# Performance work log

Hardware: AMD Instinct MI355X
Metric: run time of the kernel (lower is better)

The kernel has to match this reference:

```python
import jax, jax.numpy as jnp
import numpy as np

TAU = 0.07
COS_EPS = 1e-8   # torch F.cosine_similarity eps
L1_EPS = 1e-12   # torch F.normalize eps
MM_EPS = 1e-8    # min-max renorm eps

B, C, H, W = 64, 256, 32, 32
S, D = 512, 256


def setup_inputs() -> dict:
    key = jax.random.key(0)
    k1, k2, k3, k4 = jax.random.split(key, 4)
    scale = 1.0 / np.sqrt(D)
    return {
        "image_patches": jax.random.normal(k1, (B, C, H, W), dtype=jnp.float32),
        "text_tokens": jax.random.normal(k2, (B, S, D), dtype=jnp.float32),
        "Wv": jax.random.normal(k3, (D, D), dtype=jnp.float32) * scale,
        "bv": jnp.zeros((D,), dtype=jnp.float32),
        "Wt": jax.random.normal(k4, (D, D), dtype=jnp.float32) * scale,
        "bt": jnp.zeros((D,), dtype=jnp.float32),
    }


def _linear(x, Wgt, b):
    return x @ Wgt.T + b


def _l2n(x, axis=-1):
    n = jnp.maximum(jnp.linalg.norm(x, axis=axis, keepdims=True), COS_EPS)
    return x / n


def _sym_ce_diag(sim):
    # sim [..., N, N]; mean of -log_softmax diagonals along both class axes
    lsm_r = jax.nn.log_softmax(sim, axis=-1)
    lsm_c = jax.nn.log_softmax(sim, axis=-2)
    d_r = jnp.diagonal(lsm_r, axis1=-2, axis2=-1)
    d_c = jnp.diagonal(lsm_c, axis1=-2, axis2=-1)
    return 0.5 * (-jnp.mean(d_r) - jnp.mean(d_c))


def reference(image_patches, text_tokens, Wv, bv, Wt, bt):
    b, c, h, w = image_patches.shape
    hw = h * w
    # b c h w -> b (h w) c, then adapters
    patches = image_patches.reshape(b, c, hw).transpose(0, 2, 1)  # [b, hw, c]
    patches = _linear(patches, Wv, bv)          # [b, hw, d]
    tokens = _linear(text_tokens, Wt, bt)       # [b, s, d]

    # global embeddings: mean-pool then adapter (adapter applied twice on vision path)
    g_img = _linear(jnp.mean(patches, axis=1), Wv, bv)  # [b, d]
    g_txt = _linear(jnp.mean(tokens, axis=1), Wt, bt)   # [b, d]

    # global contrastive loss (cosine sim / tau, symmetric CE over batch)
    g_sim = (_l2n(g_img) @ _l2n(g_txt).T) / TAU         # [b, b]
    global_loss = _sym_ce_diag(g_sim)

    # fine-grained alignment
    sim = jnp.einsum('bpd,bsd->bps', patches, tokens)   # [b, hw, s]
    mn = jnp.min(sim, axis=1, keepdims=True)
    mx = jnp.max(sim, axis=1, keepdims=True)
    sim = (sim - mn) / (mx - mn + MM_EPS)
    sigma = 1.0 / hw
    sim = jnp.where(sim < sigma, 0.0, sim)
    # L1 normalize over patch dim (torch F.normalize p=1 dim=1)
    weights = sim / jnp.maximum(jnp.sum(jnp.abs(sim), axis=1, keepdims=True), L1_EPS)
    lgve = jnp.einsum('bps,bpd->bsd', weights, patches)  # [b, s, d]

    # fine-grained contrastive loss: cosine sim between grouped-vision and text tokens
    f_sim = jnp.einsum('bid,bjd->bij', _l2n(lgve), _l2n(tokens)) / TAU  # [b, s, s]
    fine_loss = _sym_ce_diag(f_sim)

    return global_loss + fine_loss
```

## Files before the change

kernel.cpp:

```cpp
#include <hip/hip_runtime.h>
#include <math.h>

#define BB   64
#define HWP  1024
#define SS   512
#define DD   256
#define TAU_INV (1.0f/0.07f)
#define SIGMA   (1.0f/1024.0f)

typedef unsigned short us;
typedef __attribute__((ext_vector_type(8))) short short8v;
typedef __attribute__((ext_vector_type(8))) unsigned short ushort8v;
typedef __attribute__((ext_vector_type(4))) float floatx4;

__device__ __forceinline__ float bf2f(us u) {
    return __uint_as_float((unsigned)u << 16);
}
__device__ __forceinline__ us f2bf(float f) {
    unsigned u = __float_as_uint(f);
    u += 0x7FFFu + ((u >> 16) & 1u);
    return (us)(u >> 16);
}
__device__ __forceinline__ void split_bf(float v, us& h, us& l) {
    h = f2bf(v);
    l = f2bf(v - bf2f(h));
}

__global__ void zero_out_k(float* out) { if (threadIdx.x == 0) out[0] = 0.0f; }

enum { OPM_F32_ROW = 0, OPM_F32_COL = 1, OPM_SPL_ROW = 2, OPM_SPL_COL = 3,
       OPM_B16_COL = 4, OPM_B16_ROW = 5, OPM_WGT_COL = 6 };
enum { OUT_F32 = 0, OUT_B16 = 1 };

#define LDSTRIDE 40

template<int MODE>
__device__ __forceinline__ void stage_tile(
    const char* p0, const char* p1, int ld, int row0, int k0,
    us* ldsH, us* ldsL, int tid,
    const float* wlo, const float* whi)
{
    if constexpr (MODE == OPM_SPL_ROW) {
        const us* ph = (const us*)p0;
        const us* pl = (const us*)p1;
        const int i = tid >> 1, ko = (tid & 1) * 16;
        const long long g = (long long)(row0 + i) * ld + k0 + ko;
        *(ushort8v*)&ldsH[i * LDSTRIDE + ko]     = *(const ushort8v*)&ph[g];
        *(ushort8v*)&ldsH[i * LDSTRIDE + ko + 8] = *(const ushort8v*)&ph[g + 8];
        *(ushort8v*)&ldsL[i * LDSTRIDE + ko]     = *(const ushort8v*)&pl[g];
        *(ushort8v*)&ldsL[i * LDSTRIDE + ko + 8] = *(const ushort8v*)&pl[g + 8];
    } else if constexpr (MODE == OPM_B16_ROW) {
        const us* ph = (const us*)p0;
        const int i = tid >> 1, ko = (tid & 1) * 16;
        const long long g = (long long)(row0 + i) * ld + k0 + ko;
        *(ushort8v*)&ldsH[i * LDSTRIDE + ko]     = *(const ushort8v*)&ph[g];
        *(ushort8v*)&ldsH[i * LDSTRIDE + ko + 8] = *(const ushort8v*)&ph[g + 8];
    } else if constexpr (MODE == OPM_F32_ROW) {
        const float* pf = (const float*)p0;
        const int i = tid >> 1, ko = (tid & 1) * 16;
        const long long g = (long long)(row0 + i) * ld + k0 + ko;
        us h16[16], l16[16];
        #pragma unroll
        for (int c = 0; c < 16; c += 4) {
            float4 v = *(const float4*)&pf[g + c];
            split_bf(v.x, h16[c+0], l16[c+0]); split_bf(v.y, h16[c+1], l16[c+1]);
            split_bf(v.z, h16[c+2], l16[c+2]); split_bf(v.w, h16[c+3], l16[c+3]);
        }
        *(ushort8v*)&ldsH[i * LDSTRIDE + ko]     = *(const ushort8v*)&h16[0];
        *(ushort8v*)&ldsH[i * LDSTRIDE + ko + 8] = *(const ushort8v*)&h16[8];
        *(ushort8v*)&ldsL[i * LDSTRIDE + ko]     = *(const ushort8v*)&l16[0];
        *(ushort8v*)&ldsL[i * LDSTRIDE + ko + 8] = *(const ushort8v*)&l16[8];
    } else if constexpr (MODE == OPM_F32_COL) {
        const float* pf = (const float*)p0;
        const int m = tid & 127, kh = (tid >> 7) * 16;
        const long long base = (long long)(k0 + kh) * ld + row0 + m;
        us vh[16], vl[16];
        #pragma unroll
        for (int kk = 0; kk < 16; ++kk)
            split_bf(pf[base + (long long)kk * ld], vh[kk], vl[kk]);
        *(ushort8v*)&ldsH[m * LDSTRIDE + kh]     = *(const ushort8v*)&vh[0];
        *(ushort8v*)&ldsH[m * LDSTRIDE + kh + 8] = *(const ushort8v*)&vh[8];
        *(ushort8v*)&ldsL[m * LDSTRIDE + kh]     = *(const ushort8v*)&vl[0];
        *(ushort8v*)&ldsL[m * LDSTRIDE + kh + 8] = *(const ushort8v*)&vl[8];
    } else if constexpr (MODE == OPM_B16_COL) {
        const us* ph = (const us*)p0;
        const int m = tid & 127, kh = (tid >> 7) * 16;
        const long long base = (long long)(k0 + kh) * ld + row0 + m;
        us v[16];
        #pragma unroll
        for (int kk = 0; kk < 16; ++kk)
            v[kk] = ph[base + (long long)kk * ld];
        *(ushort8v*)&ldsH[m * LDSTRIDE + kh]     = *(const ushort8v*)&v[0];
        *(ushort8v*)&ldsH[m * LDSTRIDE + kh + 8] = *(const ushort8v*)&v[8];
    } else if constexpr (MODE == OPM_WGT_COL) {
        const us* ph = (const us*)p0;
        const int m = tid & 127, kh = (tid >> 7) * 16;
        const float lo = wlo[row0 + m];
        const float inv = 1.0f / (whi[row0 + m] - lo + 1e-8f);
        const long long base = (long long)(k0 + kh) * ld + row0 + m;
        us v[16];
        #pragma unroll
        for (int kk = 0; kk < 16; ++kk) {
            const float w = (bf2f(ph[base + (long long)kk * ld]) - lo) * inv;
            v[kk] = (w < SIGMA) ? (us)0 : f2bf(w);
        }
        *(ushort8v*)&ldsH[m * LDSTRIDE + kh]     = *(const ushort8v*)&v[0];
        *(ushort8v*)&ldsH[m * LDSTRIDE + kh + 8] = *(const ushort8v*)&v[8];
    }
}

template<int AMODE, int BMODE, int OMODE, int EPI>
__global__ __launch_bounds__(256) void mfma_gemm(
    const void* A0, const void* A1, const void* B0, const void* B1,
    void* C0,
    int M, int N, int K, int lda, int ldb, int ldc,
    long long sA, long long sB, long long sC,
    const float* __restrict__ bias, const float* __restrict__ invm,
    const float* __restrict__ invn, float scale,
    const float* __restrict__ wlo, const float* __restrict__ whi)
{
    constexpr bool ASPL = (AMODE <= OPM_SPL_COL);
    constexpr bool BSPL = (BMODE <= OPM_SPL_COL);
    constexpr int ASZ = 128 * LDSTRIDE;
    __shared__ __align__(16) us Ah[ASZ];
    __shared__ __align__(16) us Al[ASPL ? ASZ : 8];
    __shared__ __align__(16) us Bh[ASZ];
    __shared__ __align__(16) us Bl[BSPL ? ASZ : 8];

    const int tid = threadIdx.x;
    const int w = tid >> 6, lane = tid & 63;
    const int quad = lane >> 4, l16 = lane & 15;
    const int m0 = blockIdx.x * 128, n0 = blockIdx.y * 128;
    const int b = blockIdx.z;

    const char* Ab0 = (const char*)A0 + (long long)b * sA;
    const char* Ab1 = A1 ? (const char*)A1 + (long long)b * sA : nullptr;
    const char* Bb0 = (const char*)B0 + (long long)b * sB;
    const char* Bb1 = B1 ? (const char*)B1 + (long long)b * sB : nullptr;
    const float* wloA = wlo ? wlo + (long long)b * M : nullptr;
    const float* whiA = whi ? whi + (long long)b * M : nullptr;

    floatx4 acc[2][8];
    #pragma unroll
    for (int mi = 0; mi < 2; ++mi)
        #pragma unroll
        for (int ni = 0; ni < 8; ++ni)
            acc[mi][ni] = (floatx4){0.f, 0.f, 0.f, 0.f};

    for (int k0 = 0; k0 < K; k0 += 32) {
        stage_tile<AMODE>(Ab0, Ab1, lda, m0, k0, Ah, Al, tid, wloA, whiA);
        stage_tile<BMODE>(Bb0, Bb1, ldb, n0, k0, Bh, Bl, tid, nullptr, nullptr);
        __syncthreads();

        short8v ah[2], al[2], bh[8], bl[8];
        #pragma unroll
        for (int mi = 0; mi < 2; ++mi) {
            const int r = (32 * w + 16 * mi + l16) * LDSTRIDE + quad * 8;
            ah[mi] = *(const short8v*)&Ah[r];
            if constexpr (ASPL) al[mi] = *(const short8v*)&Al[r];
        }
        #pragma unroll
        for (int ni = 0; ni < 8; ++ni) {
            const int r = (16 * ni + l16) * LDSTRIDE + quad * 8;
            bh[ni] = *(const short8v*)&Bh[r];
            if constexpr (BSPL) bl[ni] = *(const short8v*)&Bl[r];
        }
        #pragma unroll
        for (int mi = 0; mi < 2; ++mi)
            #pragma unroll
            for (int ni = 0; ni < 8; ++ni) {
                acc[mi][ni] = __builtin_amdgcn_mfma_f32_16x16x32_bf16(ah[mi], bh[ni], acc[mi][ni], 0, 0, 0);
                if constexpr (BSPL)
                    acc[mi][ni] = __builtin_amdgcn_mfma_f32_16x16x32_bf16(ah[mi], bl[ni], acc[mi][ni], 0, 0, 0);
                if constexpr (ASPL)
                    acc[mi][ni] = __builtin_amdgcn_mfma_f32_16x16x32_bf16(al[mi], bh[ni], acc[mi][ni], 0, 0, 0);
            }
        __syncthreads();
    }

    char* Cb0 = (char*)C0 + (long long)b * sC;
    #pragma unroll
    for (int mi = 0; mi < 2; ++mi)
        #pragma unroll
        for (int ni = 0; ni < 8; ++ni)
            #pragma unroll
            for (int r = 0; r < 4; ++r) {
                const int row = m0 + 32 * w + 16 * mi + quad * 4 + r;
                const int col = n0 + 16 * ni + l16;
                float v = acc[mi][ni][r];
                if constexpr (EPI == 1) v += bias[col];
                if constexpr (EPI == 2) v *= invm[b * M + row] * invn[b * N + col] * scale;
                const long long idx = (long long)row * ldc + col;
                if constexpr (OMODE == OUT_F32) ((float*)Cb0)[idx] = v;
                else                            ((us*)Cb0)[idx] = f2bf(v);
            }
}


__global__ __launch_bounds__(256) void convert_w_k(
    const float* Wv, const float* Wt, us* Wvh, us* Wvl, us* Wth, us* Wtl)
{
    const int i = blockIdx.x * 256 + threadIdx.x;
    split_bf(Wv[i], Wvh[i], Wvl[i]);
    split_bf(Wt[i], Wth[i], Wtl[i]);
}

__global__ __launch_bounds__(256) void mean_img_k(
    const float* __restrict__ img, float* __restrict__ mimg)
{
    const int row = blockIdx.x * 4 + (threadIdx.x >> 6);
    const int lane = threadIdx.x & 63;
    const float* p = img + (long long)row * 1024;
    float s = 0.f;
    #pragma unroll
    for (int c = 0; c < 4; ++c) {
        float4 v = *(const float4*)&p[(c * 64 + lane) * 4];
        s += v.x + v.y + v.z + v.w;
    }
    #pragma unroll
    for (int o = 32; o > 0; o >>= 1) s += __shfl_xor(s, o);
    if (lane == 0) mimg[row] = s * (1.0f / 1024.0f);
}

__global__ __launch_bounds__(256) void mean_text_s1(
    const float* __restrict__ text, float* __restrict__ part)
{
    const int b = blockIdx.x, ch = blockIdx.y, k = threadIdx.x;
    const float* p = text + ((long long)b * 512 + ch * 64) * 256 + k;
    float s = 0.f;
    for (int r = 0; r < 64; ++r) s += p[r * 256];
    part[(b * 8 + ch) * 256 + k] = s;
}
__global__ __launch_bounds__(256) void mean_text_s2(
    const float* __restrict__ part, float* __restrict__ mt)
{
    const int b = blockIdx.x, k = threadIdx.x;
    float s = 0.f;
    for (int c = 0; c < 8; ++c) s += part[(b * 8 + c) * 256 + k];
    mt[b * 256 + k] = s * (1.0f / 512.0f);
}

__global__ __launch_bounds__(256) void small_adapter_k(
    const float* __restrict__ x, const float* __restrict__ W,
    const float* __restrict__ bias, float* __restrict__ y)
{
    const int b = blockIdx.x, d = threadIdx.x;
    __shared__ float xs[256];
    xs[d] = x[b * 256 + d];
    __syncthreads();
    const float* w = W + (long long)d * 256;
    float s = bias[d];
    for (int k = 0; k < 256; ++k) s += xs[k] * w[k];
    y[b * 256 + d] = s;
}


__global__ __launch_bounds__(256) void inv_norm_f32_k(
    const float* __restrict__ x, float* __restrict__ inv)
{
    const int row = blockIdx.x * 4 + (threadIdx.x >> 6);
    const int lane = threadIdx.x & 63;
    float4 v = *(const float4*)&x[(long long)row * 256 + lane * 4];
    float s = v.x * v.x + v.y * v.y + v.z * v.z + v.w * v.w;
    #pragma unroll
    for (int o = 32; o > 0; o >>= 1) s += __shfl_xor(s, o);
    if (lane == 0) inv[row] = 1.0f / fmaxf(sqrtf(s), 1e-8f);
}

__global__ __launch_bounds__(256) void g_sim_k(
    const float* __restrict__ gi, const float* __restrict__ gt,
    const float* __restrict__ invI, const float* __restrict__ invT,
    float* __restrict__ gs)
{
    const int i = blockIdx.x, t = threadIdx.x;
    const int j = t >> 2, part = t & 3;
    __shared__ float a[256];
    a[t] = gi[i * 256 + t];
    __syncthreads();
    const float* bp = gt + (long long)j * 256 + part * 64;
    const float* ap = a + part * 64;
    float s = 0.f;
    #pragma unroll 16
    for (int k = 0; k < 64; ++k) s += ap[k] * bp[k];
    s += __shfl_xor(s, 1);
    s += __shfl_xor(s, 2);
    if (part == 0) gs[i * 64 + j] = s * invI[i] * invT[j] * TAU_INV;
}

__global__ __launch_bounds__(64) void g_lse_k(
    const float* __restrict__ gs, float* __restrict__ out)
{
    const int b = blockIdx.x, lane = threadIdx.x;
    const bool is_col = b >= 64;
    const int r = is_col ? b - 64 : b;
    const float v = is_col ? gs[lane * 64 + r] : gs[r * 64 + lane];
    float m = v;
    #pragma unroll
    for (int o = 32; o > 0; o >>= 1) m = fmaxf(m, __shfl_xor(m, o));
    float s = expf(v - m);
    #pragma unroll
    for (int o = 32; o > 0; o >>= 1) s += __shfl_xor(s, o);
    if (lane == 0)
        atomicAdd(out, ((m + logf(s)) - gs[r * 64 + r]) * (0.5f / 64.0f));
}

__global__ __launch_bounds__(256) void minmax_s1(
    const us* __restrict__ simW, float* __restrict__ mnp, float* __restrict__ mxp)
{
    const int bx = blockIdx.x;
    const int b = bx >> 1, s = ((bx & 1) << 8) + threadIdx.x;
    const int ch = blockIdx.y;
    const us* p = simW + ((long long)b * 1024 + ch * 128) * 512 + s;
    float lo = 1e30f, hi = -1e30f;
    for (int r = 0; r < 128; ++r) {
        const float v = bf2f(p[(long long)r * 512]);
        lo = fminf(lo, v); hi = fmaxf(hi, v);
    }
    mnp[((long long)b * 8 + ch) * 512 + s] = lo;
    mxp[((long long)b * 8 + ch) * 512 + s] = hi;
}
__global__ __launch_bounds__(256) void minmax_s2(
    const float* __restrict__ mnp, const float* __restrict__ mxp,
    float* __restrict__ mn, float* __restrict__ mx)
{
    const int bx = blockIdx.x;
    const int b = bx >> 1, s = ((bx & 1) << 8) + threadIdx.x;
    float lo = 1e30f, hi = -1e30f;
    for (int c = 0; c < 8; ++c) {
        lo = fminf(lo, mnp[((long long)b * 8 + c) * 512 + s]);
        hi = fmaxf(hi, mxp[((long long)b * 8 + c) * 512 + s]);
    }
    mn[b * 512 + s] = lo;
    mx[b * 512 + s] = hi;
}

__global__ __launch_bounds__(256) void inv_norm_b16_k(
    const us* __restrict__ x, float* __restrict__ inv)
{
    const int row = blockIdx.x * 4 + (threadIdx.x >> 6);
    const int lane = threadIdx.x & 63;
    ushort4 h = *(const ushort4*)&x[(long long)row * 256 + lane * 4];
    const float x0 = bf2f(h.x), x1 = bf2f(h.y), x2 = bf2f(h.z), x3 = bf2f(h.w);
    float s = x0 * x0 + x1 * x1 + x2 * x2 + x3 * x3;
    #pragma unroll
    for (int o = 32; o > 0; o >>= 1) s += __shfl_xor(s, o);
    if (lane == 0) inv[row] = 1.0f / fmaxf(sqrtf(s), 1e-8f);
}

__global__ __launch_bounds__(256) void row_lse_k(
    const float* __restrict__ f, float* __restrict__ out)
{
    const int w = threadIdx.x >> 6, lane = threadIdx.x & 63;
    const int r0 = blockIdx.x * 64 + w * 16;
    float accum = 0.f;
    for (int rr = 0; rr < 16; ++rr) {
        const int r = r0 + rr;
        const float* p = f + (long long)r * SS;
        float4 v0 = *(const float4*)&p[lane * 8];
        float4 v1 = *(const float4*)&p[lane * 8 + 4];
        float vals[8] = {v0.x, v0.y, v0.z, v0.w, v1.x, v1.y, v1.z, v1.w};
        float m = vals[0];
        #pragma unroll
        for (int t = 1; t < 8; ++t) m = fmaxf(m, vals[t]);
        #pragma unroll
        for (int o = 32; o > 0; o >>= 1) m = fmaxf(m, __shfl_xor(m, o));
        float s = 0.f;
        #pragma unroll
        for (int t = 0; t < 8; ++t) s += expf(vals[t] - m);
        #pragma unroll
        for (int o = 32; o > 0; o >>= 1) s += __shfl_xor(s, o);
        accum += (m + logf(s)) - p[r & (SS - 1)];
    }
    __shared__ float red[4];
    if (lane == 0) red[w] = accum;
    __syncthreads();
    if (threadIdx.x == 0)
        atomicAdd(out, (red[0] + red[1] + red[2] + red[3]) * (0.5f / (64.0f * 512.0f)));
}

__global__ __launch_bounds__(256) void col_lse_s1(
    const float* __restrict__ f, float* __restrict__ pm, float* __restrict__ ps)
{
    const int b = blockIdx.x, ch = blockIdx.y;
    const float* base = f + (long long)b * SS * SS + (long long)ch * 64 * SS;
    const int c0 = threadIdx.x * 2;
    float m0 = -1e30f, m1 = -1e30f, s0 = 0.f, s1 = 0.f;
    #pragma unroll 4
    for (int r = 0; r < 64; ++r) {
        const float2 v = *(const float2*)&base[r * SS + c0];
        const float nm0 = fmaxf(m0, v.x);
        s0 = s0 * expf(m0 - nm0) + expf(v.x - nm0);
        m0 = nm0;
        const float nm1 = fmaxf(m1, v.y);
        s1 = s1 * expf(m1 - nm1) + expf(v.y - nm1);
        m1 = nm1;
    }
    const long long o = ((long long)b * 8 + ch) * SS + c0;
    *(float2*)&pm[o] = make_float2(m0, m1);
    *(float2*)&ps[o] = make_float2(s0, s1);
}
__global__ __launch_bounds__(256) void col_lse_s2(
    const float* __restrict__ pm, const float* __restrict__ ps,
    const float* __restrict__ f, float* __restrict__ out)
{
    const int b = blockIdx.x >> 1;
    const int j = ((blockIdx.x & 1) << 8) + threadIdx.x;
    float m = -1e30f, s = 0.f;
    #pragma unroll
    for (int c = 0; c < 8; ++c) {
        const long long o = ((long long)b * 8 + c) * SS + j;
        const float cm = pm[o], cs = ps[o];
        const float nm = fmaxf(m, cm);
        s = s * expf(m - nm) + cs * expf(cm - nm);
        m = nm;
    }
    const float contrib = (m + logf(s)) - f[(long long)b * SS * SS + (long long)j * SS + j];
    __shared__ float red[256];
    red[threadIdx.x] = contrib;
    __syncthreads();
    for (int w = 128; w > 0; w >>= 1) {
        if (threadIdx.x < w) red[threadIdx.x] += red[threadIdx.x + w];
        __syncthreads();
    }
    if (threadIdx.x == 0) atomicAdd(out, red[0] * (0.5f / (64.0f * 512.0f)));
}

extern "C" void kernel_launch(void* const* d_in, const int* in_sizes, int n_in,
                              void* d_out, int out_size, void* d_ws, size_t ws_size,
                              hipStream_t stream)
{
    const float* img  = (const float*)d_in[0];
    const float* text = (const float*)d_in[1];
    const float* Wv   = (const float*)d_in[2];
    const float* bv   = (const float*)d_in[3];
    const float* Wt   = (const float*)d_in[4];
    const float* bt   = (const float*)d_in[5];
    float* out = (float*)d_out;
    char* ws = (char*)d_ws;

    us* patches = (us*)(ws + 0);
    us* tokens  = (us*)(ws + 33554432);
    us* simW    = (us*)(ws + 50331648);
    float* f_sim = (float*)(ws + 50331648);
    us* lgve    = (us*)(ws + 117440512);
    char* st = ws + 134217728;
    float* mean_img  = (float*)(st + 0);
    float* mean_text = (float*)(st + 65536);
    float* mean_pat  = (float*)(st + 131072);
    float* mean_tok  = (float*)(st + 196608);
    float* g_img     = (float*)(st + 262144);
    float* g_txt     = (float*)(st + 327680);
    float* textpart  = (float*)(st + 393216);
    float* mnp       = (float*)(st + 917504);
    float* mxp       = (float*)(st + 1966080);
    float* mnv       = (float*)(st + 3014656);
    float* mxv       = (float*)(st + 3145728);
    float* inv_l     = (float*)(st + 3276800);
    float* inv_t     = (float*)(st + 3407872);
    us* Wvh = (us*)(st + 3538944);
    us* Wvl = (us*)(st + 3670016);
    us* Wth = (us*)(st + 3801088);
    us* Wtl = (us*)(st + 3932160);
    float* inv_gi  = (float*)(st + 4063232);
    float* inv_gt  = (float*)(st + 4063744);
    float* g_simbf = (float*)(st + 4064256);
    float* col_pm  = (float*)(st + 4194304);
    float* col_ps  = (float*)(st + 5242880);

    zero_out_k<<<1, 64, 0, stream>>>(out);
    convert_w_k<<<256, 256, 0, stream>>>(Wv, Wt, Wvh, Wvl, Wth, Wtl);

    mean_img_k<<<4096, 256, 0, stream>>>(img, mean_img);
    mean_text_s1<<<dim3(64, 8), 256, 0, stream>>>(text, textpart);
    mean_text_s2<<<64, 256, 0, stream>>>(textpart, mean_text);
    small_adapter_k<<<BB, 256, 0, stream>>>(mean_img, Wv, bv, mean_pat);
    small_adapter_k<<<BB, 256, 0, stream>>>(mean_pat, Wv, bv, g_img);
    small_adapter_k<<<BB, 256, 0, stream>>>(mean_text, Wt, bt, mean_tok);
    small_adapter_k<<<BB, 256, 0, stream>>>(mean_tok, Wt, bt, g_txt);
    inv_norm_f32_k<<<16, 256, 0, stream>>>(g_img, inv_gi);
    inv_norm_f32_k<<<16, 256, 0, stream>>>(g_txt, inv_gt);
    g_sim_k<<<64, 256, 0, stream>>>(g_img, g_txt, inv_gi, inv_gt, g_simbf);
    g_lse_k<<<128, 64, 0, stream>>>(g_simbf, out);

    mfma_gemm<OPM_F32_COL, OPM_SPL_ROW, OUT_B16, 1><<<dim3(8, 2, BB), 256, 0, stream>>>(
        img, nullptr, Wvh, Wvl, patches,
        1024, 256, 256, 1024, 256, 256,
        1048576LL, 0LL, 524288LL, bv, nullptr, nullptr, 0.f, nullptr, nullptr);

    mfma_gemm<OPM_F32_ROW, OPM_SPL_ROW, OUT_B16, 1><<<dim3(4, 2, BB), 256, 0, stream>>>(
        text, nullptr, Wth, Wtl, tokens,
        512, 256, 256, 256, 256, 256,
        524288LL, 0LL, 262144LL, bt, nullptr, nullptr, 0.f, nullptr, nullptr);

    mfma_gemm<OPM_B16_ROW, OPM_B16_ROW, OUT_B16, 0><<<dim3(8, 4, BB), 256, 0, stream>>>(
        patches, nullptr, tokens, nullptr, simW,
        1024, 512, 256, 256, 256, 512,
        524288LL, 262144LL, 1048576LL, nullptr, nullptr, nullptr, 0.f, nullptr, nullptr);

    minmax_s1<<<dim3(128, 8), 256, 0, stream>>>(simW, mnp, mxp);
    minmax_s2<<<128, 256, 0, stream>>>(mnp, mxp, mnv, mxv);

    mfma_gemm<OPM_WGT_COL, OPM_B16_COL, OUT_B16, 0><<<dim3(4, 2, BB), 256, 0, stream>>>(
        simW, nullptr, patches, nullptr, lgve,
        512, 256, 1024, 512, 256, 256,
        1048576LL, 524288LL, 262144LL, nullptr, nullptr, nullptr, 0.f, mnv, mxv);

    inv_norm_b16_k<<<8192, 256, 0, stream>>>(lgve, inv_l);
    inv_norm_b16_k<<<8192, 256, 0, stream>>>(tokens, inv_t);

    mfma_gemm<OPM_B16_ROW, OPM_B16_ROW, OUT_F32, 2><<<dim3(4, 4, BB), 256, 0, stream>>>(
        lgve, nullptr, tokens, nullptr, f_sim,
        512, 512, 256, 256, 256, 512,
        262144LL, 262144LL, 1048576LL, nullptr, inv_l, inv_t, TAU_INV, nullptr, nullptr);

    row_lse_k<<<512, 256, 0, stream>>>(f_sim, out);
    col_lse_s1<<<dim3(BB, 8), 256, 0, stream>>>(f_sim, col_pm, col_ps);
    col_lse_s2<<<128, 256, 0, stream>>>(col_pm, col_ps, f_sim, out);
}
```

Baseline: 433.3 us.

## Fuse min-max and log-softmax reductions into GEMM epilogues, widen N tiles

Widens the GEMM N tile to 256 so each block reuses its A tile across more columns. The column min/max partials are computed inside the similarity GEMM epilogue, which removes a separate pass over simW. The fine-similarity GEMM no longer writes the fp32 f_sim matrix. Instead it emits per-row and per-column max/sum-exp partials plus diagonal values, and small merge kernels combine them. The cost is more accumulator registers (lower occupancy), fewer blocks per launch, and extra LDS for the reductions.

```diff
diff --git a/kernel.cpp b/kernel.cpp
--- a/kernel.cpp
+++ b/kernel.cpp
@@ -34,103 +34,109 @@
 
 #define LDSTRIDE 40
 
-template<int MODE>
+template<int MODE, int ROWS>
 __device__ __forceinline__ void stage_tile(
     const char* p0, const char* p1, int ld, int row0, int k0,
     us* ldsH, us* ldsL, int tid,
     const float* wlo, const float* whi)
 {
-    if constexpr (MODE == OPM_SPL_ROW) {
-        const us* ph = (const us*)p0;
-        const us* pl = (const us*)p1;
-        const int i = tid >> 1, ko = (tid & 1) * 16;
-        const long long g = (long long)(row0 + i) * ld + k0 + ko;
-        *(ushort8v*)&ldsH[i * LDSTRIDE + ko]     = *(const ushort8v*)&ph[g];
-        *(ushort8v*)&ldsH[i * LDSTRIDE + ko + 8] = *(const ushort8v*)&ph[g + 8];
-        *(ushort8v*)&ldsL[i * LDSTRIDE + ko]     = *(const ushort8v*)&pl[g];
-        *(ushort8v*)&ldsL[i * LDSTRIDE + ko + 8] = *(const ushort8v*)&pl[g + 8];
-    } else if constexpr (MODE == OPM_B16_ROW) {
-        const us* ph = (const us*)p0;
-        const int i = tid >> 1, ko = (tid & 1) * 16;
-        const long long g = (long long)(row0 + i) * ld + k0 + ko;
-        *(ushort8v*)&ldsH[i * LDSTRIDE + ko]     = *(const ushort8v*)&ph[g];
-        *(ushort8v*)&ldsH[i * LDSTRIDE + ko + 8] = *(const ushort8v*)&ph[g + 8];
-    } else if constexpr (MODE == OPM_F32_ROW) {
-        const float* pf = (const float*)p0;
-        const int i = tid >> 1, ko = (tid & 1) * 16;
-        const long long g = (long long)(row0 + i) * ld + k0 + ko;
-        us h16[16], l16[16];
-        #pragma unroll
-        for (int c = 0; c < 16; c += 4) {
-            float4 v = *(const float4*)&pf[g + c];
-            split_bf(v.x, h16[c+0], l16[c+0]); split_bf(v.y, h16[c+1], l16[c+1]);
-            split_bf(v.z, h16[c+2], l16[c+2]); split_bf(v.w, h16[c+3], l16[c+3]);
-        }
-        *(ushort8v*)&ldsH[i * LDSTRIDE + ko]     = *(const ushort8v*)&h16[0];
-        *(ushort8v*)&ldsH[i * LDSTRIDE + ko + 8] = *(const ushort8v*)&h16[8];
-        *(ushort8v*)&ldsL[i * LDSTRIDE + ko]     = *(const ushort8v*)&l16[0];
-        *(ushort8v*)&ldsL[i * LDSTRIDE + ko + 8] = *(const ushort8v*)&l16[8];
-    } else if constexpr (MODE == OPM_F32_COL) {
-        const float* pf = (const float*)p0;
-        const int m = tid & 127, kh = (tid >> 7) * 16;
-        const long long base = (long long)(k0 + kh) * ld + row0 + m;
-        us vh[16], vl[16];
-        #pragma unroll
-        for (int kk = 0; kk < 16; ++kk)
-            split_bf(pf[base + (long long)kk * ld], vh[kk], vl[kk]);
-        *(ushort8v*)&ldsH[m * LDSTRIDE + kh]     = *(const ushort8v*)&vh[0];
-        *(ushort8v*)&ldsH[m * LDSTRIDE + kh + 8] = *(const ushort8v*)&vh[8];
-        *(ushort8v*)&ldsL[m * LDSTRIDE + kh]     = *(const ushort8v*)&vl[0];
-        *(ushort8v*)&ldsL[m * LDSTRIDE + kh + 8] = *(const ushort8v*)&vl[8];
-    } else if constexpr (MODE == OPM_B16_COL) {
-        const us* ph = (const us*)p0;
-        const int m = tid & 127, kh = (tid >> 7) * 16;
-        const long long base = (long long)(k0 + kh) * ld + row0 + m;
-        us v[16];
-        #pragma unroll
-        for (int kk = 0; kk < 16; ++kk)
-            v[kk] = ph[base + (long long)kk * ld];
-        *(ushort8v*)&ldsH[m * LDSTRIDE + kh]     = *(const ushort8v*)&v[0];
-        *(ushort8v*)&ldsH[m * LDSTRIDE + kh + 8] = *(const ushort8v*)&v[8];
-    } else if constexpr (MODE == OPM_WGT_COL) {
-        const us* ph = (const us*)p0;
-        const int m = tid & 127, kh = (tid >> 7) * 16;
-        const float lo = wlo[row0 + m];
-        const float inv = 1.0f / (whi[row0 + m] - lo + 1e-8f);
-        const long long base = (long long)(k0 + kh) * ld + row0 + m;
-        us v[16];
-        #pragma unroll
-        for (int kk = 0; kk < 16; ++kk) {
-            const float w = (bf2f(ph[base + (long long)kk * ld]) - lo) * inv;
-            v[kk] = (w < SIGMA) ? (us)0 : f2bf(w);
-        }
-        *(ushort8v*)&ldsH[m * LDSTRIDE + kh]     = *(const ushort8v*)&v[0];
-        *(ushort8v*)&ldsH[m * LDSTRIDE + kh + 8] = *(const ushort8v*)&v[8];
-    }
-}
-
-template<int AMODE, int BMODE, int OMODE, int EPI>
+    #pragma unroll
+    for (int rr = 0; rr < ROWS / 128; ++rr) {
+        if constexpr (MODE == OPM_SPL_ROW) {
+            const us* ph = (const us*)p0;
+            const us* pl = (const us*)p1;
+            const int i = rr * 128 + (tid >> 1), ko = (tid & 1) * 16;
+            const long long g = (long long)(row0 + i) * ld + k0 + ko;
+            *(ushort8v*)&ldsH[i * LDSTRIDE + ko]     = *(const ushort8v*)&ph[g];
+            *(ushort8v*)&ldsH[i * LDSTRIDE + ko + 8] = *(const ushort8v*)&ph[g + 8];
+            *(ushort8v*)&ldsL[i * LDSTRIDE + ko]     = *(const ushort8v*)&pl[g];
+            *(ushort8v*)&ldsL[i * LDSTRIDE + ko + 8] = *(const ushort8v*)&pl[g + 8];
+        } else if constexpr (MODE == OPM_B16_ROW) {
+            const us* ph = (const us*)p0;
+            const int i = rr * 128 + (tid >> 1), ko = (tid & 1) * 16;
+            const long long g = (long long)(row0 + i) * ld + k0 + ko;
+            *(ushort8v*)&ldsH[i * LDSTRIDE + ko]     = *(const ushort8v*)&ph[g];
+            *(ushort8v*)&ldsH[i * LDSTRIDE + ko + 8] = *(const ushort8v*)&ph[g + 8];
+        } else if constexpr (MODE == OPM_F32_ROW) {
+            const float* pf = (const float*)p0;
+            const int i = rr * 128 + (tid >> 1), ko = (tid & 1) * 16;
+            const long long g = (long long)(row0 + i) * ld + k0 + ko;
+            us h16[16], l16a[16];
+            #pragma unroll
+            for (int c = 0; c < 16; c += 4) {
+                float4 v = *(const float4*)&pf[g + c];
+                split_bf(v.x, h16[c+0], l16a[c+0]); split_bf(v.y, h16[c+1], l16a[c+1]);
+                split_bf(v.z, h16[c+2], l16a[c+2]); split_bf(v.w, h16[c+3], l16a[c+3]);
+            }
+            *(ushort8v*)&ldsH[i * LDSTRIDE + ko]     = *(const ushort8v*)&h16[0];
+            *(ushort8v*)&ldsH[i * LDSTRIDE + ko + 8] = *(const ushort8v*)&h16[8];
+            *(ushort8v*)&ldsL[i * LDSTRIDE + ko]     = *(const ushort8v*)&l16a[0];
+            *(ushort8v*)&ldsL[i * LDSTRIDE + ko + 8] = *(const ushort8v*)&l16a[8];
+        } else if constexpr (MODE == OPM_F32_COL) {
+            const float* pf = (const float*)p0;
+            const int m = rr * 128 + (tid & 127), kh = (tid >> 7) * 16;
+            const long long base = (long long)(k0 + kh) * ld + row0 + m;
+            us vh[16], vl[16];
+            #pragma unroll
+            for (int kk = 0; kk < 16; ++kk)
+                split_bf(pf[base + (long long)kk * ld], vh[kk], vl[kk]);
+            *(ushort8v*)&ldsH[m * LDSTRIDE + kh]     = *(const ushort8v*)&vh[0];
+            *(ushort8v*)&ldsH[m * LDSTRIDE + kh + 8] = *(const ushort8v*)&vh[8];
+            *(ushort8v*)&ldsL[m * LDSTRIDE + kh]     = *(const ushort8v*)&vl[0];
+            *(ushort8v*)&ldsL[m * LDSTRIDE + kh + 8] = *(const ushort8v*)&vl[8];
+        } else if constexpr (MODE == OPM_B16_COL) {
+            const us* ph = (const us*)p0;
+            const int m = rr * 128 + (tid & 127), kh = (tid >> 7) * 16;
+            const long long base = (long long)(k0 + kh) * ld + row0 + m;
+            us v[16];
+            #pragma unroll
+            for (int kk = 0; kk < 16; ++kk)
+                v[kk] = ph[base + (long long)kk * ld];
+            *(ushort8v*)&ldsH[m * LDSTRIDE + kh]     = *(const ushort8v*)&v[0];
+            *(ushort8v*)&ldsH[m * LDSTRIDE + kh + 8] = *(const ushort8v*)&v[8];
+        } else if constexpr (MODE == OPM_WGT_COL) {
+            const us* ph = (const us*)p0;
+            const int m = rr * 128 + (tid & 127), kh = (tid >> 7) * 16;
+            const float lo = wlo[row0 + m];
+            const float inv = 1.0f / (whi[row0 + m] - lo + 1e-8f);
+            const long long base = (long long)(k0 + kh) * ld + row0 + m;
+            us v[16];
+            #pragma unroll
+            for (int kk = 0; kk < 16; ++kk) {
+                const float w = (bf2f(ph[base + (long long)kk * ld]) - lo) * inv;
+                v[kk] = (w < SIGMA) ? (us)0 : f2bf(w);
+            }
+            *(ushort8v*)&ldsH[m * LDSTRIDE + kh]     = *(const ushort8v*)&v[0];
+            *(ushort8v*)&ldsH[m * LDSTRIDE + kh + 8] = *(const ushort8v*)&v[8];
+        }
+    }
+}
+
+template<int AMODE, int BMODE, int OMODE, int EPI, int NT>
 __global__ __launch_bounds__(256) void mfma_gemm(
-    const void* A0, const void* A1, const void* B0, const void* B1,
-    void* C0,
+    const void* A0, const void* A1, const void* B0, const void* B1, void* C0,
     int M, int N, int K, int lda, int ldb, int ldc,
     long long sA, long long sB, long long sC,
     const float* __restrict__ bias, const float* __restrict__ invm,
     const float* __restrict__ invn, float scale,
-    const float* __restrict__ wlo, const float* __restrict__ whi)
+    const float* __restrict__ wlo, const float* __restrict__ whi,
+    float* __restrict__ aux0, float* __restrict__ aux1,
+    float* __restrict__ aux2, float* __restrict__ aux3, float* __restrict__ aux4)
 {
     constexpr bool ASPL = (AMODE <= OPM_SPL_COL);
     constexpr bool BSPL = (BMODE <= OPM_SPL_COL);
-    constexpr int ASZ = 128 * LDSTRIDE;
-    __shared__ __align__(16) us Ah[ASZ];
-    __shared__ __align__(16) us Al[ASPL ? ASZ : 8];
-    __shared__ __align__(16) us Bh[ASZ];
-    __shared__ __align__(16) us Bl[BSPL ? ASZ : 8];
+    constexpr int NF = NT / 16;
+    __shared__ __align__(16) us Ah[128 * LDSTRIDE];
+    __shared__ __align__(16) us Al[ASPL ? 128 * LDSTRIDE : 8];
+    __shared__ __align__(16) us Bh[NT * LDSTRIDE];
+    __shared__ __align__(16) us Bl[BSPL ? NT * LDSTRIDE : 8];
+    __shared__ float redm[(EPI >= 3) ? 4 * NT : 1];
+    __shared__ float reds[(EPI >= 3) ? 4 * NT : 1];
 
     const int tid = threadIdx.x;
     const int w = tid >> 6, lane = tid & 63;
     const int quad = lane >> 4, l16 = lane & 15;
-    const int m0 = blockIdx.x * 128, n0 = blockIdx.y * 128;
+    const int m0 = blockIdx.x * 128, n0 = blockIdx.y * NT;
     const int b = blockIdx.z;
 
     const char* Ab0 = (const char*)A0 + (long long)b * sA;
@@ -140,19 +146,19 @@
     const float* wloA = wlo ? wlo + (long long)b * M : nullptr;
     const float* whiA = whi ? whi + (long long)b * M : nullptr;
 
-    floatx4 acc[2][8];
+    floatx4 acc[2][NF];
     #pragma unroll
     for (int mi = 0; mi < 2; ++mi)
         #pragma unroll
-        for (int ni = 0; ni < 8; ++ni)
+        for (int ni = 0; ni < NF; ++ni)
             acc[mi][ni] = (floatx4){0.f, 0.f, 0.f, 0.f};
 
     for (int k0 = 0; k0 < K; k0 += 32) {
-        stage_tile<AMODE>(Ab0, Ab1, lda, m0, k0, Ah, Al, tid, wloA, whiA);
-        stage_tile<BMODE>(Bb0, Bb1, ldb, n0, k0, Bh, Bl, tid, nullptr, nullptr);
+        stage_tile<AMODE, 128>(Ab0, Ab1, lda, m0, k0, Ah, Al, tid, wloA, whiA);
+        stage_tile<BMODE, NT>(Bb0, Bb1, ldb, n0, k0, Bh, Bl, tid, nullptr, nullptr);
         __syncthreads();
 
-        short8v ah[2], al[2], bh[8], bl[8];
+        short8v ah[2], al[2];
         #pragma unroll
         for (int mi = 0; mi < 2; ++mi) {
             const int r = (32 * w + 16 * mi + l16) * LDSTRIDE + quad * 8;
@@ -160,40 +166,151 @@
             if constexpr (ASPL) al[mi] = *(const short8v*)&Al[r];
         }
         #pragma unroll
-        for (int ni = 0; ni < 8; ++ni) {
-            const int r = (16 * ni + l16) * LDSTRIDE + quad * 8;
-            bh[ni] = *(const short8v*)&Bh[r];
-            if constexpr (BSPL) bl[ni] = *(const short8v*)&Bl[r];
-        }
+        for (int ni = 0; ni < NF; ++ni) {
+            const int rB = (16 * ni + l16) * LDSTRIDE + quad * 8;
+            short8v bh = *(const short8v*)&Bh[rB];
+            acc[0][ni] = __builtin_amdgcn_mfma_f32_16x16x32_bf16(ah[0], bh, acc[0][ni], 0, 0, 0);
+            acc[1][ni] = __builtin_amdgcn_mfma_f32_16x16x32_bf16(ah[1], bh, acc[1][ni], 0, 0, 0);
+            if constexpr (BSPL) {
+                short8v bl = *(const short8v*)&Bl[rB];
+                acc[0][ni] = __builtin_amdgcn_mfma_f32_16x16x32_bf16(ah[0], bl, acc[0][ni], 0, 0, 0);
+                acc[1][ni] = __builtin_amdgcn_mfma_f32_16x16x32_bf16(ah[1], bl, acc[1][ni], 0, 0, 0);
+            }
+            if constexpr (ASPL) {
+                acc[0][ni] = __builtin_amdgcn_mfma_f32_16x16x32_bf16(al[0], bh, acc[0][ni], 0, 0, 0);
+                acc[1][ni] = __builtin_amdgcn_mfma_f32_16x16x32_bf16(al[1], bh, acc[1][ni], 0, 0, 0);
+            }
+        }
+        __syncthreads();
+    }
+
+    if constexpr (EPI != 4) {
+        char* Cb0 = (char*)C0 + (long long)b * sC;
         #pragma unroll
         for (int mi = 0; mi < 2; ++mi)
             #pragma unroll
-            for (int ni = 0; ni < 8; ++ni) {
-                acc[mi][ni] = __builtin_amdgcn_mfma_f32_16x16x32_bf16(ah[mi], bh[ni], acc[mi][ni], 0, 0, 0);
-                if constexpr (BSPL)
-                    acc[mi][ni] = __builtin_amdgcn_mfma_f32_16x16x32_bf16(ah[mi], bl[ni], acc[mi][ni], 0, 0, 0);
-                if constexpr (ASPL)
-                    acc[mi][ni] = __builtin_amdgcn_mfma_f32_16x16x32_bf16(al[mi], bh[ni], acc[mi][ni], 0, 0, 0);
-            }
+            for (int ni = 0; ni < NF; ++ni)
+                #pragma unroll
+                for (int r = 0; r < 4; ++r) {
+                    const int row = m0 + 32 * w + 16 * mi + quad * 4 + r;
+                    const int col = n0 + 16 * ni + l16;
+                    float v = acc[mi][ni][r];
+                    if constexpr (EPI == 1) v += bias[col];
+                    const long long idx = (long long)row * ldc + col;
+                    if constexpr (OMODE == OUT_F32) ((float*)Cb0)[idx] = v;
+                    else                            ((us*)Cb0)[idx] = f2bf(v);
+                }
+    }
+
+    if constexpr (EPI == 3) {
+        #pragma unroll
+        for (int ni = 0; ni < NF; ++ni) {
+            float lo = 1e30f, hi = -1e30f;
+            #pragma unroll
+            for (int mi = 0; mi < 2; ++mi)
+                #pragma unroll
+                for (int r = 0; r < 4; ++r) {
+                    const float vr = bf2f(f2bf(acc[mi][ni][r]));
+                    lo = fminf(lo, vr); hi = fmaxf(hi, vr);
+                }
+            lo = fminf(lo, __shfl_xor(lo, 16)); lo = fminf(lo, __shfl_xor(lo, 32));
+            hi = fmaxf(hi, __shfl_xor(hi, 16)); hi = fmaxf(hi, __shfl_xor(hi, 32));
+            if (quad == 0) {
+                redm[w * NT + 16 * ni + l16] = lo;
+                reds[w * NT + 16 * ni + l16] = hi;
+            }
+        }
         __syncthreads();
-    }
-
-    char* Cb0 = (char*)C0 + (long long)b * sC;
-    #pragma unroll
-    for (int mi = 0; mi < 2; ++mi)
-        #pragma unroll
-        for (int ni = 0; ni < 8; ++ni)
+        if (tid < NT) {
+            float lo = 1e30f, hi = -1e30f;
+            #pragma unroll
+            for (int w4 = 0; w4 < 4; ++w4) {
+                lo = fminf(lo, redm[w4 * NT + tid]);
+                hi = fmaxf(hi, reds[w4 * NT + tid]);
+            }
+            const long long o = ((long long)b * N + n0 + tid) * 8 + blockIdx.x;
+            aux0[o] = lo; aux1[o] = hi;
+        }
+    }
+
+    if constexpr (EPI == 4) {
+        float bn[NF];
+        #pragma unroll
+        for (int ni = 0; ni < NF; ++ni)
+            bn[ni] = invn[(long long)b * N + n0 + 16 * ni + l16] * scale;
+        float amv[8];
+        #pragma unroll
+        for (int mi = 0; mi < 2; ++mi)
+            #pragma unroll
+            for (int r = 0; r < 4; ++r)
+                amv[mi * 4 + r] = invm[(long long)b * M + m0 + 32 * w + 16 * mi + quad * 4 + r];
+
+        #pragma unroll
+        for (int mi = 0; mi < 2; ++mi)
             #pragma unroll
             for (int r = 0; r < 4; ++r) {
-                const int row = m0 + 32 * w + 16 * mi + quad * 4 + r;
-                const int col = n0 + 16 * ni + l16;
-                float v = acc[mi][ni][r];
-                if constexpr (EPI == 1) v += bias[col];
-                if constexpr (EPI == 2) v *= invm[b * M + row] * invn[b * N + col] * scale;
-                const long long idx = (long long)row * ldc + col;
-                if constexpr (OMODE == OUT_F32) ((float*)Cb0)[idx] = v;
-                else                            ((us*)Cb0)[idx] = f2bf(v);
-            }
+                const int grow = m0 + 32 * w + 16 * mi + quad * 4 + r;
+                float vv[NF];
+                float rm = -1e30f;
+                #pragma unroll
+                for (int ni = 0; ni < NF; ++ni) {
+                    const float v = acc[mi][ni][r] * amv[mi * 4 + r] * bn[ni];
+                    vv[ni] = v;
+                    rm = fmaxf(rm, v);
+                    if (grow == n0 + 16 * ni + l16)
+                        aux4[(long long)b * M + grow] = v;
+                }
+                #pragma unroll
+                for (int o = 8; o > 0; o >>= 1) rm = fmaxf(rm, __shfl_xor(rm, o));
+                float rs = 0.f;
+                #pragma unroll
+                for (int ni = 0; ni < NF; ++ni) rs += expf(vv[ni] - rm);
+                #pragma unroll
+                for (int o = 8; o > 0; o >>= 1) rs += __shfl_xor(rs, o);
+                if (l16 == 0) {
+                    const long long o = ((long long)b * M + grow) * 2 + blockIdx.y;
+                    aux0[o] = rm; aux1[o] = rs;
+                }
+            }
+
+        #pragma unroll
+        for (int ni = 0; ni < NF; ++ni) {
+            float va[8];
+            float cm = -1e30f;
+            #pragma unroll
+            for (int mi = 0; mi < 2; ++mi)
+                #pragma unroll
+                for (int r = 0; r < 4; ++r) {
+                    const float v = acc[mi][ni][r] * amv[mi * 4 + r] * bn[ni];
+                    va[mi * 4 + r] = v;
+                    cm = fmaxf(cm, v);
+                }
+            cm = fmaxf(cm, __shfl_xor(cm, 16));
+            cm = fmaxf(cm, __shfl_xor(cm, 32));
+            float cs = 0.f;
+            #pragma unroll
+            for (int j = 0; j < 8; ++j) cs += expf(va[j] - cm);
+            cs += __shfl_xor(cs, 16);
+            cs += __shfl_xor(cs, 32);
+            if (quad == 0) {
+                redm[w * NT + 16 * ni + l16] = cm;
+                reds[w * NT + 16 * ni + l16] = cs;
+            }
+        }
+        __syncthreads();
+        if (tid < NT) {
+            float m = -1e30f, s = 0.f;
+            #pragma unroll
+            for (int w4 = 0; w4 < 4; ++w4) {
+                const float cm = redm[w4 * NT + tid], cs = reds[w4 * NT + tid];
+                const float nm = fmaxf(m, cm);
+                s = s * expf(m - nm) + cs * expf(cm - nm);
+                m = nm;
+            }
+            const long long o = ((long long)b * N + n0 + tid) * 4 + blockIdx.x;
+            aux2[o] = m; aux3[o] = s;
+        }
+    }
 }
 
 
@@ -304,36 +421,6 @@
         atomicAdd(out, ((m + logf(s)) - gs[r * 64 + r]) * (0.5f / 64.0f));
 }
 
-__global__ __launch_bounds__(256) void minmax_s1(
-    const us* __restrict__ simW, float* __restrict__ mnp, float* __restrict__ mxp)
-{
-    const int bx = blockIdx.x;
-    const int b = bx >> 1, s = ((bx & 1) << 8) + threadIdx.x;
-    const int ch = blockIdx.y;
-    const us* p = simW + ((long long)b * 1024 + ch * 128) * 512 + s;
-    float lo = 1e30f, hi = -1e30f;
-    for (int r = 0; r < 128; ++r) {
-        const float v = bf2f(p[(long long)r * 512]);
-        lo = fminf(lo, v); hi = fmaxf(hi, v);
-    }
-    mnp[((long long)b * 8 + ch) * 512 + s] = lo;
-    mxp[((long long)b * 8 + ch) * 512 + s] = hi;
-}
-__global__ __launch_bounds__(256) void minmax_s2(
-    const float* __restrict__ mnp, const float* __restrict__ mxp,
-    float* __restrict__ mn, float* __restrict__ mx)
-{
-    const int bx = blockIdx.x;
-    const int b = bx >> 1, s = ((bx & 1) << 8) + threadIdx.x;
-    float lo = 1e30f, hi = -1e30f;
-    for (int c = 0; c < 8; ++c) {
-        lo = fminf(lo, mnp[((long long)b * 8 + c) * 512 + s]);
-        hi = fmaxf(hi, mxp[((long long)b * 8 + c) * 512 + s]);
-    }
-    mn[b * 512 + s] = lo;
-    mx[b * 512 + s] = hi;
-}
-
 __global__ __launch_bounds__(256) void inv_norm_b16_k(
     const us* __restrict__ x, float* __restrict__ inv)
 {
@@ -347,74 +434,55 @@
     if (lane == 0) inv[row] = 1.0f / fmaxf(sqrtf(s), 1e-8f);
 }
 
-__global__ __launch_bounds__(256) void row_lse_k(
-    const float* __restrict__ f, float* __restrict__ out)
-{
-    const int w = threadIdx.x >> 6, lane = threadIdx.x & 63;
-    const int r0 = blockIdx.x * 64 + w * 16;
-    float accum = 0.f;
-    for (int rr = 0; rr < 16; ++rr) {
-        const int r = r0 + rr;
-        const float* p = f + (long long)r * SS;
-        float4 v0 = *(const float4*)&p[lane * 8];
-        float4 v1 = *(const float4*)&p[lane * 8 + 4];
-        float vals[8] = {v0.x, v0.y, v0.z, v0.w, v1.x, v1.y, v1.z, v1.w};
-        float m = vals[0];
-        #pragma unroll
-        for (int t = 1; t < 8; ++t) m = fmaxf(m, vals[t]);
-        #pragma unroll
-        for (int o = 32; o > 0; o >>= 1) m = fmaxf(m, __shfl_xor(m, o));
-        float s = 0.f;
-        #pragma unroll
-        for (int t = 0; t < 8; ++t) s += expf(vals[t] - m);
-        #pragma unroll
-        for (int o = 32; o > 0; o >>= 1) s += __shfl_xor(s, o);
-        accum += (m + logf(s)) - p[r & (SS - 1)];
-    }
-    __shared__ float red[4];
-    if (lane == 0) red[w] = accum;
+
+__global__ __launch_bounds__(256) void minmax_merge_k(
+    const float* __restrict__ mnp, const float* __restrict__ mxp,
+    float* __restrict__ mn, float* __restrict__ mx)
+{
+    const int idx = blockIdx.x * 256 + threadIdx.x;
+    float lo = 1e30f, hi = -1e30f;
+    #pragma unroll
+    for (int c = 0; c < 8; ++c) {
+        lo = fminf(lo, mnp[(long long)idx * 8 + c]);
+        hi = fmaxf(hi, mxp[(long long)idx * 8 + c]);
+    }
+    mn[idx] = lo; mx[idx] = hi;
+}
+
+__global__ __launch_bounds__(256) void fine_row_merge_k(
+    const float* __restrict__ pm, const float* __restrict__ ps,
+    const float* __restrict__ diag, float* __restrict__ out)
+{
+    const int idx = blockIdx.x * 256 + threadIdx.x;
+    const float m0 = pm[(long long)idx * 2],     s0 = ps[(long long)idx * 2];
+    const float m1 = pm[(long long)idx * 2 + 1], s1 = ps[(long long)idx * 2 + 1];
+    const float nm = fmaxf(m0, m1);
+    const float S = s0 * expf(m0 - nm) + s1 * expf(m1 - nm);
+    const float contrib = (nm + logf(S)) - diag[idx];
+    __shared__ float red[256];
+    red[threadIdx.x] = contrib;
     __syncthreads();
-    if (threadIdx.x == 0)
-        atomicAdd(out, (red[0] + red[1] + red[2] + red[3]) * (0.5f / (64.0f * 512.0f)));
-}
-
-__global__ __launch_bounds__(256) void col_lse_s1(
-    const float* __restrict__ f, float* __restrict__ pm, float* __restrict__ ps)
-{
-    const int b = blockIdx.x, ch = blockIdx.y;
-    const float* base = f + (long long)b * SS * SS + (long long)ch * 64 * SS;
-    const int c0 = threadIdx.x * 2;
-    float m0 = -1e30f, m1 = -1e30f, s0 = 0.f, s1 = 0.f;
-    #pragma unroll 4
-    for (int r = 0; r < 64; ++r) {
-        const float2 v = *(const float2*)&base[r * SS + c0];
-        const float nm0 = fmaxf(m0, v.x);
-        s0 = s0 * expf(m0 - nm0) + expf(v.x - nm0);
-        m0 = nm0;
-        const float nm1 = fmaxf(m1, v.y);
-        s1 = s1 * expf(m1 - nm1) + expf(v.y - nm1);
-        m1 = nm1;
-    }
-    const long long o = ((long long)b * 8 + ch) * SS + c0;
-    *(float2*)&pm[o] = make_float2(m0, m1);
-    *(float2*)&ps[o] = make_float2(s0, s1);
-}
-__global__ __launch_bounds__(256) void col_lse_s2(
+    for (int w = 128; w > 0; w >>= 1) {
+        if (threadIdx.x < w) red[threadIdx.x] += red[threadIdx.x + w];
+        __syncthreads();
+    }
+    if (threadIdx.x == 0) atomicAdd(out, red[0] * (0.5f / (64.0f * 512.0f)));
+}
+
+__global__ __launch_bounds__(256) void fine_col_merge_k(
     const float* __restrict__ pm, const float* __restrict__ ps,
-    const float* __restrict__ f, float* __restrict__ out)
-{
-    const int b = blockIdx.x >> 1;
-    const int j = ((blockIdx.x & 1) << 8) + threadIdx.x;
+    const float* __restrict__ diag, float* __restrict__ out)
+{
+    const int idx = blockIdx.x * 256 + threadIdx.x;
     float m = -1e30f, s = 0.f;
     #pragma unroll
-    for (int c = 0; c < 8; ++c) {
-        const long long o = ((long long)b * 8 + c) * SS + j;
-        const float cm = pm[o], cs = ps[o];
+    for (int c = 0; c < 4; ++c) {
+        const float cm = pm[(long long)idx * 4 + c], cs = ps[(long long)idx * 4 + c];
         const float nm = fmaxf(m, cm);
         s = s * expf(m - nm) + cs * expf(cm - nm);
         m = nm;
     }
-    const float contrib = (m + logf(s)) - f[(long long)b * SS * SS + (long long)j * SS + j];
+    const float contrib = (m + logf(s)) - diag[idx];
     __shared__ float red[256];
     red[threadIdx.x] = contrib;
     __syncthreads();
@@ -441,7 +509,6 @@
     us* patches = (us*)(ws + 0);
     us* tokens  = (us*)(ws + 33554432);
     us* simW    = (us*)(ws + 50331648);
-    float* f_sim = (float*)(ws + 50331648);
     us* lgve    = (us*)(ws + 117440512);
     char* st = ws + 134217728;
     float* mean_img  = (float*)(st + 0);
@@ -464,8 +531,11 @@
     float* inv_gi  = (float*)(st + 4063232);
     float* inv_gt  = (float*)(st + 4063744);
     float* g_simbf = (float*)(st + 4064256);
-    float* col_pm  = (float*)(st + 4194304);
-    float* col_ps  = (float*)(st + 5242880);
+    float* pm_row  = (float*)(st + 4194304);
+    float* ps_row  = (float*)(st + 4456448);
+    float* pm_col  = (float*)(st + 4718592);
+    float* ps_col  = (float*)(st + 5242880);
+    float* diag    = (float*)(st + 5767168);
 
     zero_out_k<<<1, 64, 0, stream>>>(out);
     convert_w_k<<<256, 256, 0, stream>>>(Wv, Wt, Wvh, Wvl, Wth, Wtl);
@@ -482,38 +552,41 @@
     g_sim_k<<<64, 256, 0, stream>>>(g_img, g_txt, inv_gi, inv_gt, g_simbf);
     g_lse_k<<<128, 64, 0, stream>>>(g_simbf, out);
 
-    mfma_gemm<OPM_F32_COL, OPM_SPL_ROW, OUT_B16, 1><<<dim3(8, 2, BB), 256, 0, stream>>>(
+    mfma_gemm<OPM_F32_COL, OPM_SPL_ROW, OUT_B16, 1, 256><<<dim3(8, 1, BB), 256, 0, stream>>>(
         img, nullptr, Wvh, Wvl, patches,
         1024, 256, 256, 1024, 256, 256,
-        1048576LL, 0LL, 524288LL, bv, nullptr, nullptr, 0.f, nullptr, nullptr);
-
-    mfma_gemm<OPM_F32_ROW, OPM_SPL_ROW, OUT_B16, 1><<<dim3(4, 2, BB), 256, 0, stream>>>(
+        1048576LL, 0LL, 524288LL, bv, nullptr, nullptr, 0.f, nullptr, nullptr,
+        nullptr, nullptr, nullptr, nullptr, nullptr);
+
+    mfma_gemm<OPM_F32_ROW, OPM_SPL_ROW, OUT_B16, 1, 256><<<dim3(4, 1, BB), 256, 0, stream>>>(
         text, nullptr, Wth, Wtl, tokens,
         512, 256, 256, 256, 256, 256,
-        524288LL, 0LL, 262144LL, bt, nullptr, nullptr, 0.f, nullptr, nullptr);
-
-    mfma_gemm<OPM_B16_ROW, OPM_B16_ROW, OUT_B16, 0><<<dim3(8, 4, BB), 256, 0, stream>>>(
+        524288LL, 0LL, 262144LL, bt, nullptr, nullptr, 0.f, nullptr, nullptr,
+        nullptr, nullptr, nullptr, nullptr, nullptr);
+
+    mfma_gemm<OPM_B16_ROW, OPM_B16_ROW, OUT_B16, 3, 256><<<dim3(8, 2, BB), 256, 0, stream>>>(
         patches, nullptr, tokens, nullptr, simW,
         1024, 512, 256, 256, 256, 512,
-        524288LL, 262144LL, 1048576LL, nullptr, nullptr, nullptr, 0.f, nullptr, nullptr);
-
-    minmax_s1<<<dim3(128, 8), 256, 0, stream>>>(simW, mnp, mxp);
-    minmax_s2<<<128, 256, 0, stream>>>(mnp, mxp, mnv, mxv);
-
-    mfma_gemm<OPM_WGT_COL, OPM_B16_COL, OUT_B16, 0><<<dim3(4, 2, BB), 256, 0, stream>>>(
+        524288LL, 262144LL, 1048576LL, nullptr, nullptr, nullptr, 0.f, nullptr, nullptr,
+        mnp, mxp, nullptr, nullptr, nullptr);
+
+    minmax_merge_k<<<128, 256, 0, stream>>>(mnp, mxp, mnv, mxv);
+
+    mfma_gemm<OPM_WGT_COL, OPM_B16_COL, OUT_B16, 0, 256><<<dim3(4, 1, BB), 256, 0, stream>>>(
         simW, nullptr, patches, nullptr, lgve,
         512, 256, 1024, 512, 256, 256,
-        1048576LL, 524288LL, 262144LL, nullptr, nullptr, nullptr, 0.f, mnv, mxv);
+        1048576LL, 524288LL, 262144LL, nullptr, nullptr, nullptr, 0.f, mnv, mxv,
+        nullptr, nullptr, nullptr, nullptr, nullptr);
 
     inv_norm_b16_k<<<8192, 256, 0, stream>>>(lgve, inv_l);
     inv_norm_b16_k<<<8192, 256, 0, stream>>>(tokens, inv_t);
 
-    mfma_gemm<OPM_B16_ROW, OPM_B16_ROW, OUT_F32, 2><<<dim3(4, 4, BB), 256, 0, stream>>>(
-        lgve, nullptr, tokens, nullptr, f_sim,
+    mfma_gemm<OPM_B16_ROW, OPM_B16_ROW, OUT_B16, 4, 256><<<dim3(4, 2, BB), 256, 0, stream>>>(
+        lgve, nullptr, tokens, nullptr, nullptr,
         512, 512, 256, 256, 256, 512,
-        262144LL, 262144LL, 1048576LL, nullptr, inv_l, inv_t, TAU_INV, nullptr, nullptr);
-
-    row_lse_k<<<512, 256, 0, stream>>>(f_sim, out);
-    col_lse_s1<<<dim3(BB, 8), 256, 0, stream>>>(f_sim, col_pm, col_ps);
-    col_lse_s2<<<128, 256, 0, stream>>>(col_pm, col_ps, f_sim, out);
-}
+        262144LL, 262144LL, 0LL, nullptr, inv_l, inv_t, TAU_INV, nullptr, nullptr,
+        pm_row, ps_row, pm_col, ps_col, diag);
+
+    fine_row_merge_k<<<128, 256, 0, stream>>>(pm_row, ps_row, diag, out);
+    fine_col_merge_k<<<128, 256, 0, stream>>>(pm_col, ps_col, diag, out);
+}
```

Result: slower. 473.4 us (+9.3%).
